# Optimization experiments

Measured on AMD Instinct MI355X. Metric: run time of the kernel, lower is better.

## Reference

```python
import jax, jax.numpy as jnp
import numpy as np

S, R, DH = 8, 2, 64  # num_searches, num_retrievals, dim_head


def setup_inputs() -> dict:
    key = jax.random.key(0)
    ks = jax.random.split(key, 7)
    b, n, dim = 2, 2048, 512
    def w(k, i, o):
        return jax.random.normal(k, (i, o), dtype=jnp.float32) / np.sqrt(i)
    return {
        "x": jax.random.normal(ks[0], (b, n, dim), dtype=jnp.float32),
        "wq_s": w(ks[1], dim, S * DH),
        "wk_s": w(ks[2], dim, S * DH),
        "wv_r": w(ks[3], dim, R * DH),
        "wq_r": w(ks[4], dim, S * DH),
        "wk_ret": w(ks[5], DH, DH),
        "w_out": w(ks[6], S * DH, dim),
    }


def reference(x, wq_s, wk_s, wv_r, wq_r, wk_ret, w_out):
    b, n, dim = x.shape
    scale = DH ** -0.5
    # stage 1: search attention over sequence, per search head s
    sq = (x @ wq_s).reshape(b, n, S, DH).transpose(0, 2, 1, 3) * scale  # b s n d
    sk = (x @ wk_s).reshape(b, n, S, DH).transpose(0, 2, 1, 3)          # b s n d
    rv = (x @ wv_r).reshape(b, n, R, DH).transpose(0, 2, 1, 3)          # b r n d
    search_sim = jnp.einsum('bsid,bsjd->bsij', sq, sk)                  # b s n n
    search_attn = jax.nn.softmax(search_sim, axis=-1)
    # retrieved values: each search head attends into each retrieval's values
    retrieved = jnp.einsum('bsij,brjd->bsird', search_attn, rv)         # b s n r d
    # stage 2: retrieval composition (softmax over the r retrievals)
    rq = (x @ wq_r).reshape(b, n, S, DH).transpose(0, 2, 1, 3) * scale  # b s n d
    rk = retrieved @ wk_ret                                             # b s n r d
    retrieval_sim = jnp.einsum('bsid,bsird->bsir', rq, rk)              # b s n r
    retrieval_attn = jax.nn.softmax(retrieval_sim, axis=-1)
    out = jnp.einsum('bsir,bsird->bsid', retrieval_attn, retrieved)     # b s n d
    out = out.transpose(0, 2, 1, 3).reshape(b, n, S * DH)               # b n (s d)
    return out @ w_out
```

## Files before the change

### kernel.cpp

```cpp
#include <hip/hip_runtime.h>
#include <hip/hip_bf16.h>

#define DEV __device__ __forceinline__

typedef __attribute__((ext_vector_type(8))) short bf16x8;
typedef __attribute__((ext_vector_type(4))) float f32x4;

DEV float b2f(unsigned short u) {
    unsigned int v = ((unsigned int)u) << 16;
    float f; __builtin_memcpy(&f, &v, 4); return f;
}
DEV unsigned short f2b(float f) {
    unsigned int v; __builtin_memcpy(&v, &f, 4);
    v = (v + 0x7fffu + ((v >> 16) & 1u)) >> 16;
    return (unsigned short)v;
}
DEV unsigned short f2b_hw(float f) {
    __hip_bfloat16 h = __float2bfloat16(f);
    unsigned short u; __builtin_memcpy(&u, &h, 2); return u;
}
DEV float exp2raw(float x) { return __builtin_amdgcn_exp2f(x); }

DEV f32x4 mfma16(bf16x8 a, bf16x8 b, f32x4 c) {
    return __builtin_amdgcn_mfma_f32_16x16x32_bf16(a, b, c, 0, 0, 0);
}

DEV void stage16(const void* g, void* l) {
    __builtin_amdgcn_global_load_lds((const __attribute__((address_space(1))) void*)g,
                                     (__attribute__((address_space(3))) void*)l, 16, 0, 0);
}

#define WAIT_VM6()  asm volatile("s_waitcnt vmcnt(6)" ::: "memory")
#define WAIT_VM3()  asm volatile("s_waitcnt vmcnt(3)" ::: "memory")
#define WAIT_VM0()  asm volatile("s_waitcnt vmcnt(0)" ::: "memory")
#define WAIT_LGKM() asm volatile("s_waitcnt lgkmcnt(0)" ::: "memory")
#define BAR()       __builtin_amdgcn_s_barrier()
#define SCHED()     __builtin_amdgcn_sched_barrier(0)

constexpr float SCALE_L2E = 0.125f * 1.44269504088896340736f;

__global__ __launch_bounds__(256) void k_prep(const float* __restrict__ x,
                                              const float* __restrict__ wq_s,
                                              const float* __restrict__ wk_s,
                                              const float* __restrict__ wv_r,
                                              const float* __restrict__ wq_r,
                                              const float* __restrict__ wk_ret,
                                              const float* __restrict__ w_out,
                                              unsigned short* __restrict__ xb,
                                              unsigned short* __restrict__ wt,
                                              unsigned short* __restrict__ wot,
                                              unsigned short* __restrict__ wkt)
{
    __shared__ float tl[32][33];
    if (blockIdx.x >= 1088) {
        const int T1 = 4096 * 512;
        const int T4 = 64 * 64;
        const int total = T1 + T4;
        for (int idx = (blockIdx.x - 1088) * 256 + threadIdx.x; idx < total;
             idx += 1024 * 256) {
            if (idx < T1) xb[idx] = f2b(x[idx]);
            else          wkt[idx - T1] = f2b(wk_ret[idx - T1]);
        }
        return;
    }
    int m = blockIdx.x;
    const float* src; unsigned short* dst;
    int base, srcld, kt, nt;
    if (m < 256)      { src = wq_s;  dst = wt;  base = 0;    srcld = 512; kt = m >> 4; nt = m & 15; }
    else if (m < 512) { m -= 256; src = wk_s;  dst = wt;  base = 512;  srcld = 512; kt = m >> 4; nt = m & 15; }
    else if (m < 576) { m -= 512; src = wv_r;  dst = wt;  base = 1024; srcld = 128; kt = m >> 2; nt = m & 3; }
    else if (m < 832) { m -= 576; src = wq_r;  dst = wt;  base = 1152; srcld = 512; kt = m >> 4; nt = m & 15; }
    else              { m -= 832; src = w_out; dst = wot; base = 0;    srcld = 512; kt = m >> 4; nt = m & 15; }

    const int r = threadIdx.x >> 5, c = threadIdx.x & 31;
#pragma unroll
    for (int s = 0; s < 4; ++s) {
        int rr = r + 8 * s;
        tl[rr][c] = src[(size_t)(kt * 32 + rr) * srcld + nt * 32 + c];
    }
    __syncthreads();
#pragma unroll
    for (int s = 0; s < 4; ++s) {
        int rr = r + 8 * s;
        dst[(size_t)(base + nt * 32 + rr) * 512 + kt * 32 + c] = f2b(tl[c][rr]);
    }
}

template<int EPI>
__global__ __launch_bounds__(256, 2) void k_gemm(const unsigned short* __restrict__ A,
                                                 const unsigned short* __restrict__ Bt,
                                                 unsigned short* __restrict__ qs,
                                                 unsigned short* __restrict__ ks,
                                                 unsigned short* __restrict__ rqb,
                                                 unsigned short* __restrict__ vt,
                                                 float* __restrict__ out)
{
    __shared__ unsigned char ab_lds[49152];

    const int tid = threadIdx.x;
    const int lane = tid & 63, wid = tid >> 6;
    const int lr = lane & 15, lg = lane >> 4;
    const int wr = wid >> 1, wc = wid & 1;
    const int brow0 = blockIdx.x * 128;
    const int bcol0 = blockIdx.y * 64;

    const int sub = lane >> 3;
    const int chk = lane & 7;
    const int scs = chk ^ sub;

    const f32x4 z = {0.f, 0.f, 0.f, 0.f};
    f32x4 acc[4][2];
#pragma unroll
    for (int m = 0; m < 4; ++m)
#pragma unroll
        for (int n = 0; n < 2; ++n) acc[m][n] = z;

    const unsigned short* Ab = A + (size_t)brow0 * 512;

    auto STAGE = [&](int buf, int k0) {
        unsigned char* ab = ab_lds + buf * 16384;
        unsigned char* bb = ab_lds + 32768 + buf * 8192;
#pragma unroll
        for (int ii = 0; ii < 4; ++ii) {
            int r0 = wid * 32 + ii * 8;
            const unsigned short* g = Ab + (size_t)(r0 + sub) * 512 + k0 + scs * 8;
            stage16(g, ab + r0 * 128);
        }
#pragma unroll
        for (int ii = 0; ii < 2; ++ii) {
            int r0 = wid * 16 + ii * 8;
            const unsigned short* g = Bt + (size_t)(bcol0 + r0 + sub) * 512 + k0 + scs * 8;
            stage16(g, bb + r0 * 128);
        }
    };

    auto COMPUTE = [&](const int cur) {
        const unsigned char* ab = ab_lds + cur * 16384;
        const unsigned char* bb = ab_lds + 32768 + cur * 8192;
#pragma unroll
        for (int ksb = 0; ksb < 2; ++ksb) {
            const int c = ksb * 4 + lg;
            bf16x8 bfr[2];
#pragma unroll
            for (int n = 0; n < 2; ++n) {
                int row = wc * 32 + n * 16 + lr;
                bfr[n] = *(const bf16x8*)(bb + row * 128 + ((c ^ (row & 7)) << 4));
            }
#pragma unroll
            for (int m = 0; m < 4; ++m) {
                int row = wr * 64 + m * 16 + lr;
                bf16x8 af = *(const bf16x8*)(ab + row * 128 + ((c ^ (row & 7)) << 4));
                acc[m][0] = mfma16(af, bfr[0], acc[m][0]);
                acc[m][1] = mfma16(af, bfr[1], acc[m][1]);
            }
        }
    };

    STAGE(0, 0);
#pragma unroll 1
    for (int it = 0; it < 3; ++it) {
        STAGE(1, (2 * it + 1) * 64);
        WAIT_VM6(); BAR(); SCHED();
        COMPUTE(0);
        WAIT_LGKM(); SCHED(); BAR(); SCHED();
        STAGE(0, (2 * it + 2) * 64);
        WAIT_VM6(); BAR(); SCHED();
        COMPUTE(1);
        WAIT_LGKM(); SCHED(); BAR(); SCHED();
    }
    STAGE(1, 7 * 64);
    WAIT_VM6(); BAR(); SCHED();
    COMPUTE(0);
    WAIT_LGKM(); SCHED(); BAR(); SCHED();
    WAIT_VM0(); BAR(); SCHED();
    COMPUTE(1);

#pragma unroll
    for (int m = 0; m < 4; ++m) {
#pragma unroll
        for (int n = 0; n < 2; ++n) {
#pragma unroll
            for (int i = 0; i < 4; ++i) {
                int gr = brow0 + wr * 64 + m * 16 + lg * 4 + i;
                int gc = bcol0 + wc * 32 + n * 16 + lr;
                float v = acc[m][n][i];
                if (EPI == 1) {
                    out[(size_t)gr * 512 + gc] = v;
                } else {
                    int b = gr >> 11, in = gr & 2047;
                    if (gc < 512) {
                        int s = gc >> 6, d = gc & 63;
                        qs[((b * 8 + s) * 2048 + in) * 64 + d] = f2b(v * SCALE_L2E);
                    } else if (gc < 1024) {
                        int cgc = gc - 512; int s = cgc >> 6, d = cgc & 63;
                        ks[((b * 8 + s) * 2048 + in) * 64 + d] = f2b(v);
                    } else if (gc < 1152) {
                        int cgc = gc - 1024;
                        vt[(b * 128 + cgc) * 2048 + in] = f2b(v);
                    } else {
                        int cgc = gc - 1152; int s = cgc >> 6, d = cgc & 63;
                        rqb[((b * 8 + s) * 2048 + in) * 64 + d] = f2b(v * SCALE_L2E);
                    }
                }
            }
        }
    }
}

__global__ __launch_bounds__(512, 4) void k_attn(const unsigned short* __restrict__ qs,
                                                 const unsigned short* __restrict__ ks,
                                                 const unsigned short* __restrict__ rqb,
                                                 const unsigned short* __restrict__ vt,
                                                 const unsigned short* __restrict__ wkt,
                                                 unsigned short* __restrict__ ob)
{
    __shared__ unsigned char kv_lds[49152];

    const int tid = threadIdx.x;
    const int lane = tid & 63, wid = tid >> 6;
    const int lr = lane & 15, lg = lane >> 4;
    const int qsub = wid & 3, h = wid >> 2;
    const int bid = blockIdx.x;
    const int bs = bid >> 5, qt = bid & 31;
    const int gb = bs >> 3, gs = bs & 7;
    const int qrow0 = qt * 64 + qsub * 16;

    const int sub = lane >> 3;

    const unsigned short* qbase = qs + ((size_t)bs * 2048 + qrow0 + lr) * 64 + lg * 8;
    const bf16x8 q0 = *(const bf16x8*)(qbase);
    const bf16x8 q1 = *(const bf16x8*)(qbase + 32);

    const unsigned short* kbase = ks + (size_t)bs * 131072;
    const unsigned short* vbase = vt + (size_t)gb * 262144;

    const f32x4 z = {0.f, 0.f, 0.f, 0.f};

    float m_r = -3.0e38f;
    float acc_l = 0.f;
    f32x4 acc[8];
#pragma unroll
    for (int c8 = 0; c8 < 8; ++c8) acc[c8] = z;

    const int fbb = ((lr >> 2) & 1) << 2;
    const int f0  = (lr & 3) ^ fbb;
    const int f1  = ((lr & 3) | 4) ^ fbb;
    const int rk0 = h * 32 + (lr >> 2) * 8 + (lr & 3);
    const int rk1 = rk0 + 4;
    const int ko0a = rk0 * 128 + ((lg ^ f0) << 4);
    const int ko0b = rk0 * 128 + (((lg + 4) ^ f0) << 4);
    const int ko1a = rk1 * 128 + ((lg ^ f1) << 4);
    const int ko1b = rk1 * 128 + (((lg + 4) ^ f1) << 4);
    const int vx = lr * 128 + (((h * 4 + lg) ^ (lr & 7) ^ (((lr >> 3) & 1) << 2)) << 4);

    const unsigned short* sp[3];
    int step[3], loff[3];
#pragma unroll
    for (int j = 0; j < 3; ++j) {
        int s = wid * 3 + j;
        int scs = (lane & 7) ^ sub ^ ((s & 1) << 2);
        if (s < 8) { sp[j] = kbase + (size_t)(s * 8 + sub) * 64 + scs * 8;          step[j] = 4096; }
        else       { sp[j] = vbase + (size_t)((s - 8) * 8 + sub) * 2048 + scs * 8;  step[j] = 64;   }
        loff[j] = s * 1024;
    }

    auto STAGE = [&](const int buf) {
        unsigned char* base = kv_lds + buf * 24576;
#pragma unroll
        for (int j = 0; j < 3; ++j) {
            stage16(sp[j], base + loff[j]);
            sp[j] += step[j];
        }
    };

    auto COMPUTE = [&](const int cur) {
        const unsigned char* kb = kv_lds + cur * 24576;
        const unsigned char* vb = kb + 8192;

        f32x4 s[2];
        __builtin_amdgcn_s_setprio(1);
        {
            bf16x8 kf0 = *(const bf16x8*)(kb + ko0a);
            bf16x8 kf1 = *(const bf16x8*)(kb + ko0b);
            f32x4 t = z;
            t = mfma16(kf0, q0, t);
            t = mfma16(kf1, q1, t);
            s[0] = t;
        }
        {
            bf16x8 kf0 = *(const bf16x8*)(kb + ko1a);
            bf16x8 kf1 = *(const bf16x8*)(kb + ko1b);
            f32x4 t = z;
            t = mfma16(kf0, q0, t);
            t = mfma16(kf1, q1, t);
            s[1] = t;
        }
        __builtin_amdgcn_s_setprio(0);

        float lm = fmaxf(fmaxf(fmaxf(s[0][0], s[0][1]), fmaxf(s[0][2], s[0][3])),
                         fmaxf(fmaxf(s[1][0], s[1][1]), fmaxf(s[1][2], s[1][3])));
        if (__any(lm > m_r + 8.0f)) {
            float mx = fmaxf(lm, __shfl_xor(lm, 16));
            mx = fmaxf(mx, __shfl_xor(mx, 32));
            float m_new = fmaxf(m_r, mx);
            float alpha = exp2raw(m_r - m_new);
            float al[4];
#pragma unroll
            for (int i = 0; i < 4; ++i) al[i] = __shfl(alpha, lg * 4 + i, 16);
#pragma unroll
            for (int c8 = 0; c8 < 8; ++c8)
#pragma unroll
                for (int i = 0; i < 4; ++i) acc[c8][i] *= al[i];
            acc_l *= alpha;
            m_r = m_new;
        }

        float p[8];
#pragma unroll
        for (int a = 0; a < 2; ++a)
#pragma unroll
            for (int i = 0; i < 4; ++i)
                p[a * 4 + i] = exp2raw(s[a][i] - m_r);
        acc_l += ((p[0] + p[1]) + (p[2] + p[3])) + ((p[4] + p[5]) + (p[6] + p[7]));
        unsigned int pu[4];
#pragma unroll
        for (int t2 = 0; t2 < 4; ++t2)
            asm("v_cvt_pk_bf16_f32 %0, %1, %2" : "=v"(pu[t2]) : "v"(p[2 * t2]), "v"(p[2 * t2 + 1]));
        bf16x8 pa;
        __builtin_memcpy(&pa, pu, 16);

        __builtin_amdgcn_s_setprio(1);
#pragma unroll
        for (int c8 = 0; c8 < 8; ++c8) {
            bf16x8 vf = *(const bf16x8*)(vb + c8 * 2048 + vx);
            acc[c8] = mfma16(pa, vf, acc[c8]);
        }
        __builtin_amdgcn_s_setprio(0);
    };

    STAGE(0);

#pragma unroll 1
    for (int it = 0; it < 15; ++it) {
        STAGE(1);
        WAIT_VM3(); BAR(); SCHED();
        COMPUTE(0);
        WAIT_LGKM(); SCHED(); BAR(); SCHED();
        STAGE(0);
        WAIT_VM3(); BAR(); SCHED();
        COMPUTE(1);
        WAIT_LGKM(); SCHED(); BAR(); SCHED();
    }
    STAGE(1);
    WAIT_VM3(); BAR(); SCHED();
    COMPUTE(0);
    WAIT_LGKM(); SCHED(); BAR(); SCHED();
    WAIT_VM0(); BAR(); SCHED();
    COMPUTE(1);

    float l2 = acc_l + __shfl_xor(acc_l, 16);
    float l_row = l2 + __shfl_xor(l2, 32);

    __syncthreads();
    float* mrg = (float*)kv_lds;
    float* ml  = (float*)(kv_lds + 33792);
    if (h == 1) {
#pragma unroll
        for (int c8 = 0; c8 < 8; ++c8)
#pragma unroll
            for (int i = 0; i < 4; ++i)
                mrg[(qsub * 16 + lg * 4 + i) * 132 + c8 * 16 + lr] = acc[c8][i];
        if (lane < 16) {
            ml[(qsub * 16 + lane) * 2 + 0] = m_r;
            ml[(qsub * 16 + lane) * 2 + 1] = l_row;
        }
    }
    __syncthreads();
    if (h == 1) return;

    float m_own[4], l_own[4];
#pragma unroll
    for (int i = 0; i < 4; ++i) {
        m_own[i] = __shfl(m_r,  lg * 4 + i, 16);
        l_own[i] = __shfl(l_row, lg * 4 + i, 16);
    }

    float inv[4];
    f32x4 accM[8];
#pragma unroll
    for (int i = 0; i < 4; ++i) {
        float m_b = ml[(qsub * 16 + lg * 4 + i) * 2 + 0];
        float l_b = ml[(qsub * 16 + lg * 4 + i) * 2 + 1];
        float m_new = fmaxf(m_own[i], m_b);
        float fa = exp2raw(m_own[i] - m_new);
        float fb2 = exp2raw(m_b - m_new);
        inv[i] = 1.0f / (l_own[i] * fa + l_b * fb2);
#pragma unroll
        for (int c8 = 0; c8 < 8; ++c8)
            accM[c8][i] = acc[c8][i] * fa + mrg[(qsub * 16 + lg * 4 + i) * 132 + c8 * 16 + lr] * fb2;
    }

    const unsigned short* rqbase = rqb + ((size_t)bs * 2048 + qrow0 + lr) * 64 + lg * 8;
    const bf16x8 rq0 = *(const bf16x8*)(rqbase);
    const bf16x8 rq1 = *(const bf16x8*)(rqbase + 32);

    f32x4 Tt[4];
#pragma unroll
    for (int ct = 0; ct < 4; ++ct) {
        bf16x8 wb0 = *(const bf16x8*)(wkt + (ct * 16 + lr) * 64 + lg * 8);
        bf16x8 wb1 = *(const bf16x8*)(wkt + (ct * 16 + lr) * 64 + 32 + lg * 8);
        f32x4 t = z;
        t = mfma16(rq0, wb0, t);
        t = mfma16(rq1, wb1, t);
        Tt[ct] = t;
    }

    float w0v[4], w1v[4];
#pragma unroll
    for (int i = 0; i < 4; ++i) {
        float s0 = 0.f, s1 = 0.f;
#pragma unroll
        for (int ct = 0; ct < 4; ++ct) {
            s0 += Tt[ct][i] * accM[ct][i];
            s1 += Tt[ct][i] * accM[4 + ct][i];
        }
        s0 *= inv[i]; s1 *= inv[i];
        s0 += __shfl_xor(s0, 1, 16); s1 += __shfl_xor(s1, 1, 16);
        s0 += __shfl_xor(s0, 2, 16); s1 += __shfl_xor(s1, 2, 16);
        s0 += __shfl_xor(s0, 4, 16); s1 += __shfl_xor(s1, 4, 16);
        s0 += __shfl_xor(s0, 8, 16); s1 += __shfl_xor(s1, 8, 16);
        float mm = fmaxf(s0, s1);
        float e0 = exp2raw(s0 - mm), e1 = exp2raw(s1 - mm);
        float inw = 1.0f / (e0 + e1);
        w0v[i] = e0 * inw; w1v[i] = e1 * inw;
    }

#pragma unroll
    for (int ct = 0; ct < 4; ++ct) {
#pragma unroll
        for (int i = 0; i < 4; ++i) {
            float o = (w0v[i] * accM[ct][i] + w1v[i] * accM[4 + ct][i]) * inv[i];
            ob[((size_t)gb * 2048 + qrow0 + lg * 4 + i) * 512 + gs * 64 + ct * 16 + lr] = f2b_hw(o);
        }
    }
}

extern "C" void kernel_launch(void* const* d_in, const int* in_sizes, int n_in,
                              void* d_out, int out_size, void* d_ws, size_t ws_size,
                              hipStream_t stream)
{
    (void)in_sizes; (void)n_in; (void)out_size; (void)ws_size;
    const float* x      = (const float*)d_in[0];
    const float* wq_s   = (const float*)d_in[1];
    const float* wk_s   = (const float*)d_in[2];
    const float* wv_r   = (const float*)d_in[3];
    const float* wq_r   = (const float*)d_in[4];
    const float* wk_ret = (const float*)d_in[5];
    const float* w_out  = (const float*)d_in[6];

    char* ws = (char*)d_ws;
    unsigned short* xb  = (unsigned short*)(ws + 0);
    unsigned short* wt  = (unsigned short*)(ws + 4194304);
    unsigned short* qsb = (unsigned short*)(ws + 5898240);
    unsigned short* ksb = (unsigned short*)(ws + 10092544);
    unsigned short* rqb = (unsigned short*)(ws + 14286848);
    unsigned short* vtb = (unsigned short*)(ws + 18481152);
    unsigned short* obb = (unsigned short*)(ws + 19529728);
    unsigned short* wot = (unsigned short*)(ws + 23724032);
    unsigned short* wkt = (unsigned short*)(ws + 24248320);

    hipLaunchKernelGGL(k_prep, dim3(2112), dim3(256), 0, stream,
                       x, wq_s, wk_s, wv_r, wq_r, wk_ret, w_out, xb, wt, wot, wkt);
    hipLaunchKernelGGL((k_gemm<0>), dim3(32, 26), dim3(256), 0, stream,
                       xb, wt, qsb, ksb, rqb, vtb, (float*)nullptr);
    hipLaunchKernelGGL(k_attn, dim3(512), dim3(512), 0, stream,
                       qsb, ksb, rqb, vtb, wkt, obb);
    hipLaunchKernelGGL((k_gemm<1>), dim3(32, 8), dim3(256), 0, stream,
                       obb, wot, (unsigned short*)nullptr, (unsigned short*)nullptr,
                       (unsigned short*)nullptr, (unsigned short*)nullptr, (float*)d_out);
}
```

Before: 74.86 us.

## Template GEMM tile sizes, vectorize x conversion, simplify attention LDS swizzle

The GEMM kernel is templated on per-wave M/N fragment counts. The projection GEMM now uses 128x128 tiles over a 32x13 grid, and the output GEMM uses 64x64 tiles over a 64x8 grid, with the vmcnt wait depth adjusted to match. The x-to-bf16 conversion in the prep kernel now works on float4 loads and 4-wide stores instead of scalars. The attention kernel's LDS XOR swizzle is simplified to a plain row&7 pattern, which may change bank-conflict behaviour. Larger tiles improve reuse but raise register and LDS use, and smaller output tiles add parallelism.

```diff
diff --git a/kernel.cpp b/kernel.cpp
--- a/kernel.cpp
+++ b/kernel.cpp
@@ -5,6 +5,7 @@
 
 typedef __attribute__((ext_vector_type(8))) short bf16x8;
 typedef __attribute__((ext_vector_type(4))) float f32x4;
+typedef __attribute__((ext_vector_type(4))) unsigned short u16x4;
 
 DEV float b2f(unsigned short u) {
     unsigned int v = ((unsigned int)u) << 16;
@@ -30,7 +31,8 @@
                                      (__attribute__((address_space(3))) void*)l, 16, 0, 0);
 }
 
-#define WAIT_VM6()  asm volatile("s_waitcnt vmcnt(6)" ::: "memory")
+#define WAIT_VM8()  asm volatile("s_waitcnt vmcnt(8)" ::: "memory")
+#define WAIT_VM4()  asm volatile("s_waitcnt vmcnt(4)" ::: "memory")
 #define WAIT_VM3()  asm volatile("s_waitcnt vmcnt(3)" ::: "memory")
 #define WAIT_VM0()  asm volatile("s_waitcnt vmcnt(0)" ::: "memory")
 #define WAIT_LGKM() asm volatile("s_waitcnt lgkmcnt(0)" ::: "memory")
@@ -53,13 +55,21 @@
 {
     __shared__ float tl[32][33];
     if (blockIdx.x >= 1088) {
-        const int T1 = 4096 * 512;
-        const int T4 = 64 * 64;
-        const int total = T1 + T4;
-        for (int idx = (blockIdx.x - 1088) * 256 + threadIdx.x; idx < total;
-             idx += 1024 * 256) {
-            if (idx < T1) xb[idx] = f2b(x[idx]);
-            else          wkt[idx - T1] = f2b(wk_ret[idx - T1]);
+        const int U1 = 4096 * 512 / 4;
+        const int U2 = 64 * 64 / 4;
+        const int total = U1 + U2;
+        for (int u = (blockIdx.x - 1088) * 256 + threadIdx.x; u < total;
+             u += 1024 * 256) {
+            if (u < U1) {
+                float4 v = ((const float4*)x)[u];
+                u16x4 o = { f2b(v.x), f2b(v.y), f2b(v.z), f2b(v.w) };
+                *(u16x4*)(xb + u * 4) = o;
+            } else {
+                int t = u - U1;
+                float4 v = ((const float4*)wk_ret)[t];
+                u16x4 o = { f2b(v.x), f2b(v.y), f2b(v.z), f2b(v.w) };
+                *(u16x4*)(wkt + t * 4) = o;
+            }
         }
         return;
     }
@@ -86,7 +96,7 @@
     }
 }
 
-template<int EPI>
+template<int EPI, int MB, int NB>
 __global__ __launch_bounds__(256, 2) void k_gemm(const unsigned short* __restrict__ A,
                                                  const unsigned short* __restrict__ Bt,
                                                  unsigned short* __restrict__ qs,
@@ -95,94 +105,103 @@
                                                  unsigned short* __restrict__ vt,
                                                  float* __restrict__ out)
 {
-    __shared__ unsigned char ab_lds[49152];
+    constexpr int ABYTES = 2 * MB * 16 * 128;
+    constexpr int BBYTES = 2 * NB * 16 * 128;
+    __shared__ unsigned char ab_lds[2 * (ABYTES + BBYTES)];
 
     const int tid = threadIdx.x;
     const int lane = tid & 63, wid = tid >> 6;
     const int lr = lane & 15, lg = lane >> 4;
     const int wr = wid >> 1, wc = wid & 1;
-    const int brow0 = blockIdx.x * 128;
-    const int bcol0 = blockIdx.y * 64;
+    const int brow0 = blockIdx.x * (2 * MB * 16);
+    const int bcol0 = blockIdx.y * (2 * NB * 16);
 
     const int sub = lane >> 3;
     const int chk = lane & 7;
     const int scs = chk ^ sub;
 
     const f32x4 z = {0.f, 0.f, 0.f, 0.f};
-    f32x4 acc[4][2];
-#pragma unroll
-    for (int m = 0; m < 4; ++m)
-#pragma unroll
-        for (int n = 0; n < 2; ++n) acc[m][n] = z;
+    f32x4 acc[MB][NB];
+#pragma unroll
+    for (int m = 0; m < MB; ++m)
+#pragma unroll
+        for (int n = 0; n < NB; ++n) acc[m][n] = z;
 
     const unsigned short* Ab = A + (size_t)brow0 * 512;
 
     auto STAGE = [&](int buf, int k0) {
-        unsigned char* ab = ab_lds + buf * 16384;
-        unsigned char* bb = ab_lds + 32768 + buf * 8192;
-#pragma unroll
-        for (int ii = 0; ii < 4; ++ii) {
-            int r0 = wid * 32 + ii * 8;
+        unsigned char* ab = ab_lds + buf * ABYTES;
+        unsigned char* bb = ab_lds + 2 * ABYTES + buf * BBYTES;
+#pragma unroll
+        for (int ii = 0; ii < MB; ++ii) {
+            int r0 = (wid * MB + ii) * 8;
             const unsigned short* g = Ab + (size_t)(r0 + sub) * 512 + k0 + scs * 8;
             stage16(g, ab + r0 * 128);
         }
 #pragma unroll
-        for (int ii = 0; ii < 2; ++ii) {
-            int r0 = wid * 16 + ii * 8;
+        for (int ii = 0; ii < NB; ++ii) {
+            int r0 = (wid * NB + ii) * 8;
             const unsigned short* g = Bt + (size_t)(bcol0 + r0 + sub) * 512 + k0 + scs * 8;
             stage16(g, bb + r0 * 128);
         }
     };
 
     auto COMPUTE = [&](const int cur) {
-        const unsigned char* ab = ab_lds + cur * 16384;
-        const unsigned char* bb = ab_lds + 32768 + cur * 8192;
+        const unsigned char* ab = ab_lds + cur * ABYTES;
+        const unsigned char* bb = ab_lds + 2 * ABYTES + cur * BBYTES;
 #pragma unroll
         for (int ksb = 0; ksb < 2; ++ksb) {
             const int c = ksb * 4 + lg;
-            bf16x8 bfr[2];
-#pragma unroll
-            for (int n = 0; n < 2; ++n) {
-                int row = wc * 32 + n * 16 + lr;
+            bf16x8 bfr[NB];
+#pragma unroll
+            for (int n = 0; n < NB; ++n) {
+                int row = wc * (NB * 16) + n * 16 + lr;
                 bfr[n] = *(const bf16x8*)(bb + row * 128 + ((c ^ (row & 7)) << 4));
             }
 #pragma unroll
-            for (int m = 0; m < 4; ++m) {
-                int row = wr * 64 + m * 16 + lr;
+            for (int m = 0; m < MB; ++m) {
+                int row = wr * (MB * 16) + m * 16 + lr;
                 bf16x8 af = *(const bf16x8*)(ab + row * 128 + ((c ^ (row & 7)) << 4));
-                acc[m][0] = mfma16(af, bfr[0], acc[m][0]);
-                acc[m][1] = mfma16(af, bfr[1], acc[m][1]);
+#pragma unroll
+                for (int n = 0; n < NB; ++n)
+                    acc[m][n] = mfma16(af, bfr[n], acc[m][n]);
             }
         }
+    };
+
+    auto WAIT_STEADY = [&]() {
+        if constexpr (MB + NB == 4) { WAIT_VM4(); }
+        else if constexpr (MB + NB == 8) { WAIT_VM8(); }
+        else { WAIT_VM0(); }
     };
 
     STAGE(0, 0);
 #pragma unroll 1
     for (int it = 0; it < 3; ++it) {
         STAGE(1, (2 * it + 1) * 64);
-        WAIT_VM6(); BAR(); SCHED();
+        WAIT_STEADY(); BAR(); SCHED();
         COMPUTE(0);
         WAIT_LGKM(); SCHED(); BAR(); SCHED();
         STAGE(0, (2 * it + 2) * 64);
-        WAIT_VM6(); BAR(); SCHED();
+        WAIT_STEADY(); BAR(); SCHED();
         COMPUTE(1);
         WAIT_LGKM(); SCHED(); BAR(); SCHED();
     }
     STAGE(1, 7 * 64);
-    WAIT_VM6(); BAR(); SCHED();
+    WAIT_STEADY(); BAR(); SCHED();
     COMPUTE(0);
     WAIT_LGKM(); SCHED(); BAR(); SCHED();
     WAIT_VM0(); BAR(); SCHED();
     COMPUTE(1);
 
 #pragma unroll
-    for (int m = 0; m < 4; ++m) {
-#pragma unroll
-        for (int n = 0; n < 2; ++n) {
+    for (int m = 0; m < MB; ++m) {
+#pragma unroll
+        for (int n = 0; n < NB; ++n) {
 #pragma unroll
             for (int i = 0; i < 4; ++i) {
-                int gr = brow0 + wr * 64 + m * 16 + lg * 4 + i;
-                int gc = bcol0 + wc * 32 + n * 16 + lr;
+                int gr = brow0 + wr * (MB * 16) + m * 16 + lg * 4 + i;
+                int gc = bcol0 + wc * (NB * 16) + n * 16 + lr;
                 float v = acc[m][n][i];
                 if (EPI == 1) {
                     out[(size_t)gr * 512 + gc] = v;
@@ -226,6 +245,7 @@
     const int qrow0 = qt * 64 + qsub * 16;
 
     const int sub = lane >> 3;
+    const int scs = (lane & 7) ^ sub;
 
     const unsigned short* qbase = qs + ((size_t)bs * 2048 + qrow0 + lr) * 64 + lg * 8;
     const bf16x8 q0 = *(const bf16x8*)(qbase);
@@ -242,23 +262,19 @@
 #pragma unroll
     for (int c8 = 0; c8 < 8; ++c8) acc[c8] = z;
 
-    const int fbb = ((lr >> 2) & 1) << 2;
-    const int f0  = (lr & 3) ^ fbb;
-    const int f1  = ((lr & 3) | 4) ^ fbb;
     const int rk0 = h * 32 + (lr >> 2) * 8 + (lr & 3);
     const int rk1 = rk0 + 4;
-    const int ko0a = rk0 * 128 + ((lg ^ f0) << 4);
-    const int ko0b = rk0 * 128 + (((lg + 4) ^ f0) << 4);
-    const int ko1a = rk1 * 128 + ((lg ^ f1) << 4);
-    const int ko1b = rk1 * 128 + (((lg + 4) ^ f1) << 4);
-    const int vx = lr * 128 + (((h * 4 + lg) ^ (lr & 7) ^ (((lr >> 3) & 1) << 2)) << 4);
+    const int ko0a = rk0 * 128 + ((lg ^ (rk0 & 7)) << 4);
+    const int ko0b = rk0 * 128 + (((lg + 4) ^ (rk0 & 7)) << 4);
+    const int ko1a = rk1 * 128 + ((lg ^ (rk1 & 7)) << 4);
+    const int ko1b = rk1 * 128 + (((lg + 4) ^ (rk1 & 7)) << 4);
+    const int vx = lr * 128 + (((h * 4 + lg) ^ (lr & 7)) << 4);
 
     const unsigned short* sp[3];
     int step[3], loff[3];
 #pragma unroll
     for (int j = 0; j < 3; ++j) {
         int s = wid * 3 + j;
-        int scs = (lane & 7) ^ sub ^ ((s & 1) << 2);
         if (s < 8) { sp[j] = kbase + (size_t)(s * 8 + sub) * 64 + scs * 8;          step[j] = 4096; }
         else       { sp[j] = vbase + (size_t)((s - 8) * 8 + sub) * 2048 + scs * 8;  step[j] = 64;   }
         loff[j] = s * 1024;
@@ -471,11 +487,11 @@
 
     hipLaunchKernelGGL(k_prep, dim3(2112), dim3(256), 0, stream,
                        x, wq_s, wk_s, wv_r, wq_r, wk_ret, w_out, xb, wt, wot, wkt);
-    hipLaunchKernelGGL((k_gemm<0>), dim3(32, 26), dim3(256), 0, stream,
+    hipLaunchKernelGGL((k_gemm<0, 4, 4>), dim3(32, 13), dim3(256), 0, stream,
                        xb, wt, qsb, ksb, rqb, vtb, (float*)nullptr);
     hipLaunchKernelGGL(k_attn, dim3(512), dim3(512), 0, stream,
                        qsb, ksb, rqb, vtb, wkt, obb);
-    hipLaunchKernelGGL((k_gemm<1>), dim3(32, 8), dim3(256), 0, stream,
+    hipLaunchKernelGGL((k_gemm<1, 2, 2>), dim3(64, 8), dim3(256), 0, stream,
                        obb, wot, (unsigned short*)nullptr, (unsigned short*)nullptr,
                        (unsigned short*)nullptr, (unsigned short*)nullptr, (float*)d_out);
 }
```

Result: faster. 70.45 us (-5.9%).
